# Kernel optimization log

Measured on AMD Instinct MI355X. Metric: run time of the kernel, lower is better.

Reference implementation:

```python
import jax, jax.numpy as jnp
import numpy as np

T_DEC = 60  # decoder steps, hard-coded in the original forward

def _conv1d(x, w, b):
    # x: [B, C_in, L], w: [C_out, C_in, K] -> [B, C_out, L-K+1] (valid conv)
    y = jax.lax.conv_general_dilated(x, w, window_strides=(1,), padding='VALID',
                                     dimension_numbers=('NCH', 'OIH', 'NCH'))
    return y + b[None, :, None]

def _lstm_cell(x, h, c, wih, whh, bih, bhh):
    # PyTorch LSTM cell, gate order i, f, g, o
    g = x @ wih.T + h @ whh.T + (bih + bhh)
    i, f, gg, o = jnp.split(g, 4, axis=-1)
    c = jax.nn.sigmoid(f) * c + jax.nn.sigmoid(i) * jnp.tanh(gg)
    h = jax.nn.sigmoid(o) * jnp.tanh(c)
    return h, c

def _lstm_seq(xs, wih, whh, bih, bhh, reverse=False):
    # xs: [B, T, D] -> [B, T, H], zero initial state (PyTorch default)
    B, H = xs.shape[0], whh.shape[1]
    xs_t = jnp.swapaxes(xs, 0, 1)
    if reverse:
        xs_t = xs_t[::-1]
    def step(carry, x):
        h, c = carry
        h, c = _lstm_cell(x, h, c, wih, whh, bih, bhh)
        return (h, c), h
    init = (jnp.zeros((B, H), xs.dtype), jnp.zeros((B, H), xs.dtype))
    _, hs = jax.lax.scan(step, init, xs_t)
    if reverse:
        hs = hs[::-1]
    return jnp.swapaxes(hs, 0, 1)

def setup_inputs():
    key = jax.random.key(0)
    B, L, D_in, H, D_out = 64, 4096, 64, 256, 128
    C1, C2, C3 = 8, 16, 32
    ks = jax.random.split(key, 32)
    it = iter(ks)
    def p(shape, scale=0.1):
        return jax.random.normal(next(it), shape, jnp.float32) * scale
    inp = {}
    inp['x'] = jax.random.normal(next(it), (B, L, D_in), jnp.float32)
    inp['conv_w1'] = p((C1, D_in, 4)); inp['conv_b1'] = p((C1,))
    inp['conv_w2'] = p((C2, C1, 8));  inp['conv_b2'] = p((C2,))
    inp['conv_w3'] = p((C3, C2, 16)); inp['conv_b3'] = p((C3,))
    inp['attn_w'] = p((H, C3)); inp['attn_b'] = p((H,))
    inp['dec1_wih'] = p((2, 4 * H, C3)); inp['dec1_whh'] = p((2, 4 * H, H))
    inp['dec1_bih'] = p((2, 4 * H));     inp['dec1_bhh'] = p((2, 4 * H))
    inp['dec2_wih0'] = p((2, 4 * H, 2 * H)); inp['dec2_whh0'] = p((2, 4 * H, H))
    inp['dec2_bih0'] = p((2, 4 * H));        inp['dec2_bhh0'] = p((2, 4 * H))
    inp['dec2_wih1'] = p((2, 4 * H, 2 * H)); inp['dec2_whh1'] = p((2, 4 * H, H))
    inp['dec2_bih1'] = p((2, 4 * H));        inp['dec2_bhh1'] = p((2, 4 * H))
    inp['out_w'] = p((D_out, 2 * H)); inp['out_b'] = p((D_out,))
    return inp

def reference(x, conv_w1, conv_b1, conv_w2, conv_b2, conv_w3, conv_b3,
              attn_w, attn_b, dec1_wih, dec1_whh, dec1_bih, dec1_bhh,
              dec2_wih0, dec2_whh0, dec2_bih0, dec2_bhh0,
              dec2_wih1, dec2_whh1, dec2_bih1, dec2_bhh1, out_w, out_b):
    # Eval mode: all dropouts are identity.
    h = jnp.swapaxes(x, 1, 2)  # [B, D_in, L]
    h = jax.nn.relu(_conv1d(h, conv_w1, conv_b1))
    h = jax.nn.relu(_conv1d(h, conv_w2, conv_b2))
    h = jax.nn.relu(_conv1d(h, conv_w3, conv_b3))
    enc = jnp.swapaxes(h, 1, 2)  # [B, Lp, 32], Lp = L - 25
    keys_t = jnp.einsum('blc,hc->bhl', enc, attn_w) + attn_b[None, :, None]  # [B, H, Lp]
    B, H = x.shape[0], attn_w.shape[0]

    def dec1(wih, whh, bih, bhh):
        def step(carry, _):
            hh, cc = carry
            align = jnp.einsum('bh,bhl->bl', hh, keys_t)   # attention scores over Lp
            a = jax.nn.softmax(align, axis=-1)
            ctx = jnp.einsum('bl,blc->bc', a, enc)         # context [B, 32]
            hh, cc = _lstm_cell(ctx, hh, cc, wih, whh, bih, bhh)
            return (hh, cc), hh
        init = (jnp.zeros((B, H), x.dtype), jnp.zeros((B, H), x.dtype))
        _, hs = jax.lax.scan(step, init, None, length=T_DEC)
        return jnp.swapaxes(hs, 0, 1)  # [B, 60, H]

    fwd = dec1(dec1_wih[0], dec1_whh[0], dec1_bih[0], dec1_bhh[0])
    # the bkwd branch writes step i into slot 60-i-1, i.e. time-reversed outputs
    bkwd = dec1(dec1_wih[1], dec1_whh[1], dec1_bih[1], dec1_bhh[1])[:, ::-1]
    d2in = jnp.concatenate([fwd, bkwd], axis=-1)  # [B, 60, 2H]
    l0 = jnp.concatenate([
        _lstm_seq(d2in, dec2_wih0[0], dec2_whh0[0], dec2_bih0[0], dec2_bhh0[0]),
        _lstm_seq(d2in, dec2_wih0[1], dec2_whh0[1], dec2_bih0[1], dec2_bhh0[1], reverse=True)], axis=-1)
    l1 = jnp.concatenate([
        _lstm_seq(l0, dec2_wih1[0], dec2_whh1[0], dec2_bih1[0], dec2_bhh1[0]),
        _lstm_seq(l0, dec2_wih1[1], dec2_whh1[1], dec2_bih1[1], dec2_bhh1[1], reverse=True)], axis=-1)
    return l1 @ out_w.T + out_b  # [B, 60, D_out]
```

## Files before the change

### kernel.cpp

```cpp
#include <hip/hip_runtime.h>

#define B_    64
#define L1C   4093
#define L2C   4086
#define L3C   4071
#define TDEC  60

static __device__ __forceinline__ float sigf(float x){ return 1.f/(1.f + __expf(-x)); }

typedef _Float16 h2_t __attribute__((ext_vector_type(2)));
union U2H { unsigned u; h2_t h; };

static __device__ __forceinline__ unsigned pkh2(float a, float b){
  U2H r; r.h[0] = (_Float16)a; r.h[1] = (_Float16)b; return r.u;
}
static __device__ __forceinline__ float dot2f(unsigned w, unsigned h, float acc){
  U2H a; a.u = w; U2H b; b.u = h;
#if __has_builtin(__builtin_amdgcn_fdot2)
  return __builtin_amdgcn_fdot2(a.h, b.h, acc, false);
#else
  acc = fmaf((float)a.h[0], (float)b.h[0], acc);
  acc = fmaf((float)a.h[1], (float)b.h[1], acc);
  return acc;
#endif
}

#define DOT8(g, wv, hv) \
  g = dot2f(wv.x, hv.x, g); g = dot2f(wv.y, hv.y, g); \
  g = dot2f(wv.z, hv.z, g); g = dot2f(wv.w, hv.w, g);

template<int CTRL>
static __device__ __forceinline__ float dppadd(float x){
  int y = __builtin_amdgcn_update_dpp(0, __float_as_int(x), CTRL, 0xf, 0xf, true);
  return x + __int_as_float(y);
}

template<int CIN,int COUT,int KW>
__global__ __launch_bounds__(256) void k_conv(
    const float* __restrict__ in, const float* __restrict__ w,
    const float* __restrict__ bias, float* __restrict__ outp,
    int Lin_, int Lout_)
{
  int g = blockIdx.x*256 + threadIdx.x;
  int bi = g / Lout_;
  int l  = g - bi*Lout_;
  if (bi >= B_) return;
  float acc[COUT];
#pragma unroll
  for (int o=0;o<COUT;o++) acc[o] = bias[o];
  const float* ip = in + ((size_t)bi*Lin_ + l)*CIN;
  for (int k=0;k<KW;k++){
#pragma unroll
    for (int i4=0;i4<CIN/4;i4++){
      float4 xv = *(const float4*)(ip + k*CIN + i4*4);
#pragma unroll
      for (int c=0;c<4;c++){
        float xs = (&xv.x)[c];
        int i = i4*4+c;
#pragma unroll
        for (int o=0;o<COUT;o++)
          acc[o] = fmaf(xs, w[(o*CIN + i)*KW + k], acc[o]);
      }
    }
  }
  float* op = outp + ((size_t)bi*Lout_ + l)*COUT;
#pragma unroll
  for (int o=0;o<COUT;o++) op[o] = fmaxf(acc[o],0.f);
}

__global__ __launch_bounds__(256) void k_conv3q(
    const float* __restrict__ in, const float* __restrict__ w,
    const float* __restrict__ bias, uint4* __restrict__ encq,
    float* __restrict__ encs, int Lin_, int Lout_)
{
  int g = blockIdx.x*256 + threadIdx.x;
  int bi = g / Lout_;
  int l  = g - bi*Lout_;
  if (bi >= B_) return;
  float acc[32];
#pragma unroll
  for (int o=0;o<32;o++) acc[o] = bias[o];
  const float* ip = in + ((size_t)bi*Lin_ + l)*16;
  for (int k=0;k<16;k++){
#pragma unroll
    for (int i4=0;i4<4;i4++){
      float4 xv = *(const float4*)(ip + k*16 + i4*4);
#pragma unroll
      for (int c=0;c<4;c++){
        float xs = (&xv.x)[c];
        int i = i4*4+c;
#pragma unroll
        for (int o=0;o<32;o++)
          acc[o] = fmaf(xs, w[(o*16 + i)*16 + k], acc[o]);
      }
    }
  }
  float mx = 0.f;
#pragma unroll
  for (int o=0;o<32;o++){ acc[o] = fmaxf(acc[o],0.f); mx = fmaxf(mx, acc[o]); }
  float scale = mx * (1.f/255.f);
  float inv = (mx > 0.f) ? (255.f/mx) : 0.f;
  unsigned qs[8];
#pragma unroll
  for (int q8=0;q8<8;q8++){
    unsigned q0 = (unsigned)(acc[q8*4+0]*inv + 0.5f);
    unsigned q1 = (unsigned)(acc[q8*4+1]*inv + 0.5f);
    unsigned q2 = (unsigned)(acc[q8*4+2]*inv + 0.5f);
    unsigned q3 = (unsigned)(acc[q8*4+3]*inv + 0.5f);
    qs[q8] = q0 | (q1<<8) | (q2<<16) | (q3<<24);
  }
  uint4* op = encq + ((size_t)bi*Lout_ + l)*2;
  op[0] = make_uint4(qs[0],qs[1],qs[2],qs[3]);
  op[1] = make_uint4(qs[4],qs[5],qs[6],qs[7]);
  encs[(size_t)bi*Lout_ + l] = scale;
}

__global__ __launch_bounds__(256) void k_packwh(
    const float* __restrict__ w, uint4* __restrict__ wT, int K)
{
  int gid = blockIdx.x*256 + threadIdx.x;
  int per = (K/8)*1024;
  int d = gid / per, rem = gid - d*per;
  int j8 = rem >> 10, row = rem & 1023;
  const float* src = w + ((size_t)d*1024 + row)*K + j8*8;
  float4 a = *(const float4*)src;
  float4 b = *(const float4*)(src+4);
  uint4 o;
  o.x = pkh2(a.x, a.y);
  o.y = pkh2(a.z, a.w);
  o.z = pkh2(b.x, b.y);
  o.w = pkh2(b.z, b.w);
  wT[gid] = o;
}

#define CVT8(r, qv) \
  r[0]=(float)( qv.x      & 255u); r[1]=(float)((qv.x>>8 ) & 255u); \
  r[2]=(float)((qv.x>>16) & 255u); r[3]=(float)((qv.x>>24)       ); \
  r[4]=(float)( qv.y      & 255u); r[5]=(float)((qv.y>>8 ) & 255u); \
  r[6]=(float)((qv.y>>16) & 255u); r[7]=(float)((qv.y>>24)       );

__global__ __launch_bounds__(1024) void k_dec1g(
    const uint4* __restrict__ encq,
    const float* __restrict__ encs,
    const float* __restrict__ attn_w,
    const uint4* __restrict__ wihT,
    const uint4* __restrict__ whhT,
    const float* __restrict__ bih, const float* __restrict__ bhh,
    float* __restrict__ d2in)
{
  int b = blockIdx.x, d = blockIdx.y, tid = threadIdx.x;
  int c = tid & 3, rb = tid >> 2;

  __shared__ __align__(16) uint2 encQ2[16384];
  __shared__ float sls[4096];
  __shared__ __align__(16) float hls[256];
  __shared__ __align__(16) unsigned h2pk[128];
  __shared__ __align__(16) unsigned ctxh[16];
  __shared__ float vl[32];
  __shared__ float maxenc[32];
  __shared__ float Msh;
  __shared__ float red[1024];
  __shared__ float scr[512];
  __shared__ float gls[1024];

  {
    const uint4* src = encq + (size_t)b*L3C*2;
    uint4* dst = (uint4*)encQ2;
    for (int i = tid; i < 8192; i += 1024)
      dst[i] = (i < L3C*2) ? src[i] : make_uint4(0,0,0,0);
    const float* ss = encs + (size_t)b*L3C;
    for (int i = tid; i < 4096; i += 1024)
      sls[i] = (i < L3C) ? ss[i] : 0.f;
  }
  if (tid < 256) hls[tid] = 0.f;
  if (tid < 128) h2pk[tid] = 0u;
  float creg = 0.f;
  float bsum = bih[(size_t)d*1024 + tid] + bhh[(size_t)d*1024 + tid];
  const uint4* whp = whhT + (size_t)d*32768;
  __syncthreads();

  {
    float mc[8];
#pragma unroll
    for (int j=0;j<8;j++) mc[j] = 0.f;
#pragma unroll
    for (int k=0;k<16;k++){
      int l = rb + 256*k;
      uint2 qv = encQ2[l*4 + c];
      float sl = sls[l];
      float r[8]; CVT8(r, qv)
#pragma unroll
      for (int j=0;j<8;j++) mc[j] = fmaxf(mc[j], r[j]*sl);
    }
#pragma unroll
    for (int off=4; off<=32; off<<=1){
#pragma unroll
      for (int j=0;j<8;j++) mc[j] = fmaxf(mc[j], __shfl_xor(mc[j], off));
    }
    int wid = tid >> 6;
    if ((tid&63) < 4){
#pragma unroll
      for (int j=0;j<8;j++) scr[wid*32 + c*8 + j] = mc[j];
    }
    __syncthreads();
    if (tid < 32){
      float mm = 0.f;
#pragma unroll
      for (int w=0;w<16;w++) mm = fmaxf(mm, scr[w*32 + tid]);
      maxenc[tid] = mm;
    }
    __syncthreads();
  }

  for (int t=0; t<TDEC; t++){
    {
      int cc = tid & 31, part = tid >> 5;
      const float* wp = attn_w + (size_t)(part*8)*32 + cc;
      float s = 0.f;
#pragma unroll
      for (int k=0;k<8;k++) s = fmaf(hls[part*8+k], wp[k*32], s);
      red[tid] = s;
    }
    __syncthreads();
    if (tid < 32){
      float v = 0.f;
#pragma unroll
      for (int q=0;q<32;q++) v += red[q*32 + tid];
      vl[tid] = v;
      float mt = maxenc[tid] * fmaxf(v, 0.f);
#pragma unroll
      for (int off=1; off<32; off<<=1) mt += __shfl_xor(mt, off);
      if (tid==0) Msh = mt;
    }
    __syncthreads();

    float vreg[8];
#pragma unroll
    for (int j=0;j<8;j++) vreg[j] = vl[c*8 + j];
    float M = Msh;
    float ssum = 0.f;
    float acc[8];
#pragma unroll
    for (int j=0;j<8;j++) acc[j] = 0.f;
    float g = bsum;
#pragma unroll 4
    for (int k=0;k<16;k++){
      uint4 wv0 = whp[(2*k  )*1024 + tid];
      uint4 wv1 = whp[(2*k+1)*1024 + tid];
      int l = rb + 256*k;
      uint2 qv = encQ2[l*4 + c];
      float sl = sls[l];
      float r[8]; CVT8(r, qv)
      float s = 0.f;
#pragma unroll
      for (int j=0;j<8;j++) s = fmaf(r[j], vreg[j], s);
      s = dppadd<0xB1>(s);
      s = dppadd<0x4E>(s);
      s *= sl;
      if (l >= L3C) s = -3.0e38f;
      float e = __expf(s - M);
      ssum += e;
      float em = e * sl;
#pragma unroll
      for (int j=0;j<8;j++) acc[j] = fmaf(em, r[j], acc[j]);
      uint4 hv0 = *(const uint4*)&h2pk[(2*k  )*4];
      uint4 hv1 = *(const uint4*)&h2pk[(2*k+1)*4];
      DOT8(g, wv0, hv0)
      DOT8(g, wv1, hv1)
    }
    ssum = dppadd<0x124>(ssum); ssum = dppadd<0x128>(ssum);
    ssum += __shfl_xor(ssum, 16); ssum += __shfl_xor(ssum, 32);
#pragma unroll
    for (int j=0;j<8;j++){
      acc[j] = dppadd<0x124>(acc[j]); acc[j] = dppadd<0x128>(acc[j]);
      acc[j] += __shfl_xor(acc[j], 16); acc[j] += __shfl_xor(acc[j], 32);
    }
    int wid = tid >> 6;
    if ((tid&63) < 4){
#pragma unroll
      for (int j=0;j<8;j++) scr[wid*32 + c*8 + j] = acc[j];
    }
    if ((tid&63)==0) red[wid] = ssum;
    __syncthreads();
    if (tid < 32){
      float S = 0.f, s2 = 0.f;
#pragma unroll
      for (int w=0;w<16;w++){ S += red[w]; s2 += scr[w*32 + tid]; }
      float cv = s2 / S;
      float co = __shfl_xor(cv, 1);
      if (!(tid&1)) ctxh[tid>>1] = pkh2(cv, co);
    }
    __syncthreads();

#pragma unroll
    for (int c8=0;c8<4;c8++){
      uint4 wv = wihT[(size_t)d*4096 + c8*1024 + tid];
      uint4 hv = *(const uint4*)&ctxh[c8*4];
      DOT8(g, wv, hv)
    }
    gls[tid] = g;
    __syncthreads();
    if (tid < 256){
      float ii = sigf(gls[tid]);
      float ff = sigf(gls[256+tid]);
      float gg = tanhf(gls[512+tid]);
      float oo = sigf(gls[768+tid]);
      creg = fmaf(ff, creg, ii*gg);
      float hn = oo * tanhf(creg);
      hls[tid] = hn;
      float ho = __shfl_xor(hn, 1);
      if (!(tid&1)) h2pk[tid>>1] = pkh2(hn, ho);
      int tout = d ? (59 - t) : t;
      d2in[((size_t)b*60 + tout)*512 + d*256 + tid] = hn;
    }
    __syncthreads();
  }
}

__global__ __launch_bounds__(256) void k_gemm(
    const float* __restrict__ A, const float* __restrict__ W,
    float* __restrict__ C, const float* __restrict__ b1, const float* __restrict__ b2,
    int K, int ldc, size_t sW, size_t sC, int sB)
{
  int m0 = blockIdx.x * 128, n0 = blockIdx.y * 128, z = blockIdx.z;
  const float* Wz = W + (size_t)z*sW;
  float* Cz = C + (size_t)z*sC;
  const float* b1z = b1 + (size_t)z*sB;
  const float* b2z = b2 ? (b2 + (size_t)z*sB) : nullptr;
  __shared__ __align__(16) float As[16][132];
  __shared__ __align__(16) float Bs[16][132];
  int tid = threadIdx.x;
  int tx = tid & 15, ty = tid >> 4;
  int r = tid >> 2, c4 = tid & 3;
  float acc[8][8] = {};
  for (int k0=0; k0<K; k0+=16){
#pragma unroll
    for (int h=0; h<2; h++){
      int rr = r + h*64;
      float4 av = *(const float4*)(A  + (size_t)(m0+rr)*K + k0 + c4*4);
      float4 bv = *(const float4*)(Wz + (size_t)(n0+rr)*K + k0 + c4*4);
      As[c4*4+0][rr]=av.x; As[c4*4+1][rr]=av.y; As[c4*4+2][rr]=av.z; As[c4*4+3][rr]=av.w;
      Bs[c4*4+0][rr]=bv.x; Bs[c4*4+1][rr]=bv.y; Bs[c4*4+2][rr]=bv.z; Bs[c4*4+3][rr]=bv.w;
    }
    __syncthreads();
#pragma unroll
    for (int kk=0; kk<16; kk++){
      float a[8], bb[8];
      *(float4*)&a[0]  = *(const float4*)&As[kk][ty*8];
      *(float4*)&a[4]  = *(const float4*)&As[kk][ty*8+4];
      *(float4*)&bb[0] = *(const float4*)&Bs[kk][tx*8];
      *(float4*)&bb[4] = *(const float4*)&Bs[kk][tx*8+4];
#pragma unroll
      for (int i=0;i<8;i++)
#pragma unroll
        for (int j=0;j<8;j++)
          acc[i][j] = fmaf(a[i], bb[j], acc[i][j]);
    }
    __syncthreads();
  }
  float bb1[8];
#pragma unroll
  for (int j=0;j<8;j++){
    int n = n0 + tx*8 + j;
    bb1[j] = b1z[n] + (b2z ? b2z[n] : 0.f);
  }
#pragma unroll
  for (int i=0;i<8;i++){
    int m = m0 + ty*8 + i;
    float o[8];
#pragma unroll
    for (int j=0;j<8;j++) o[j] = acc[i][j] + bb1[j];
    *(float4*)(Cz + (size_t)m*ldc + n0 + tx*8)     = *(const float4*)&o[0];
    *(float4*)(Cz + (size_t)m*ldc + n0 + tx*8 + 4) = *(const float4*)&o[4];
  }
}

__global__ __launch_bounds__(1024) void k_rec2(
    const float* __restrict__ xg,
    const uint4* __restrict__ wT,
    float* __restrict__ out)
{
  int b = blockIdx.x, d = blockIdx.y, tid = threadIdx.x;
  __shared__ __align__(16) unsigned h2pk[128];
  __shared__ float gls[1024];
  float c = 0.f;
  if (tid < 128) h2pk[tid] = 0u;
  const uint4* wp = wT + (size_t)d*32*1024;
  uint4 wpre[16];
#pragma unroll
  for (int j=0;j<16;j++) wpre[j] = wp[j*1024 + tid];
  const float* xp = xg + (((size_t)d*64 + b)*60)*1024;
  __syncthreads();
  for (int step=0; step<TDEC; step++){
    int t = d ? (TDEC-1-step) : step;
    float g = xp[(size_t)t*1024 + tid];
#pragma unroll
    for (int j8=0;j8<16;j8++){
      uint4 hv = *(const uint4*)&h2pk[j8*4];
      DOT8(g, wpre[j8], hv)
    }
#pragma unroll 4
    for (int j8=16;j8<32;j8++){
      uint4 wv = wp[j8*1024 + tid];
      uint4 hv = *(const uint4*)&h2pk[j8*4];
      DOT8(g, wv, hv)
    }
    gls[tid] = g;
    __syncthreads();
    if (tid < 256){
      float ii = sigf(gls[tid]);
      float ff = sigf(gls[256+tid]);
      float gg = tanhf(gls[512+tid]);
      float oo = sigf(gls[768+tid]);
      c = fmaf(ff, c, ii*gg);
      float hn = oo * tanhf(c);
      float ho = __shfl_xor(hn, 1);
      if (!(tid&1)) h2pk[tid>>1] = pkh2(hn, ho);
      out[((size_t)b*60 + t)*512 + d*256 + tid] = hn;
    }
    __syncthreads();
  }
}

extern "C" void kernel_launch(void* const* d_in, const int* in_sizes, int n_in,
                              void* d_out, int out_size, void* d_ws, size_t ws_size,
                              hipStream_t stream) {
  const float* x      = (const float*)d_in[0];
  const float* cw1    = (const float*)d_in[1];
  const float* cb1    = (const float*)d_in[2];
  const float* cw2    = (const float*)d_in[3];
  const float* cb2    = (const float*)d_in[4];
  const float* cw3    = (const float*)d_in[5];
  const float* cb3    = (const float*)d_in[6];
  const float* attn_w = (const float*)d_in[7];
  const float* d1_wih = (const float*)d_in[9];
  const float* d1_whh = (const float*)d_in[10];
  const float* d1_bih = (const float*)d_in[11];
  const float* d1_bhh = (const float*)d_in[12];
  const float* w2_ih0 = (const float*)d_in[13];
  const float* w2_hh0 = (const float*)d_in[14];
  const float* b2_ih0 = (const float*)d_in[15];
  const float* b2_hh0 = (const float*)d_in[16];
  const float* w2_ih1 = (const float*)d_in[17];
  const float* w2_hh1 = (const float*)d_in[18];
  const float* b2_ih1 = (const float*)d_in[19];
  const float* b2_hh1 = (const float*)d_in[20];
  const float* out_w  = (const float*)d_in[21];
  const float* out_b  = (const float*)d_in[22];

  char* ws = (char*)d_ws;
  size_t off = 0;
  uint4* encq = (uint4*)(ws + off);
  float* encs = (float*)(ws + off + 8338432);
  off += 16675840;
  size_t off_h1 = off;
  float* h1buf = (float*)(ws + off); off += 8382464;
  float* h2buf = (float*)(ws + off); off += 16736256;
  float* d2in  = (float*)(ws + off_h1);
  float* l0    = (float*)(ws + off_h1 + 7864320);
  float* l1    = (float*)(ws + off_h1 + 15728640);
  uint4* wT    = (uint4*)(ws + off_h1 + 23592960);
  float* xg    = (float*)(ws + off); off += 31457280;
  uint4* d1whhT = (uint4*)xg;
  uint4* d1wihT = (uint4*)((char*)xg + 1048576);
  (void)ws_size; (void)in_sizes; (void)n_in; (void)out_size;

  k_packwh<<<256,256,0,stream>>>(d1_whh, d1whhT, 256);
  k_packwh<<<32, 256,0,stream>>>(d1_wih, d1wihT, 32);

  int g1 = (B_*L1C + 255)/256;
  k_conv<64,8,4><<<g1,256,0,stream>>>(x, cw1, cb1, h1buf, 4096, L1C);
  int g2 = (B_*L2C + 255)/256;
  k_conv<8,16,8><<<g2,256,0,stream>>>(h1buf, cw2, cb2, h2buf, L1C, L2C);
  int g3 = (B_*L3C + 255)/256;
  k_conv3q<<<g3,256,0,stream>>>(h2buf, cw3, cb3, encq, encs, L2C, L3C);

  k_dec1g<<<dim3(64,2),1024,0,stream>>>(encq, encs, attn_w, d1wihT, d1whhT,
                                        d1_bih, d1_bhh, d2in);

  k_packwh<<<256,256,0,stream>>>(w2_hh0, wT, 256);
  k_gemm<<<dim3(30,8,2),256,0,stream>>>(d2in, w2_ih0, xg, b2_ih0, b2_hh0,
                                        512, 1024, (size_t)1024*512, (size_t)3840*1024, 1024);
  k_rec2<<<dim3(64,2),1024,0,stream>>>(xg, wT, l0);
  k_packwh<<<256,256,0,stream>>>(w2_hh1, wT, 256);
  k_gemm<<<dim3(30,8,2),256,0,stream>>>(l0, w2_ih1, xg, b2_ih1, b2_hh1,
                                        512, 1024, (size_t)1024*512, (size_t)3840*1024, 1024);
  k_rec2<<<dim3(64,2),1024,0,stream>>>(xg, wT, l1);
  k_gemm<<<dim3(30,1,1),256,0,stream>>>(l1, out_w, (float*)d_out, out_b, nullptr,
                                        512, 128, 0, 0, 0);
}
```

Baseline: 1.606 ms.

## Stage conv input windows in shared memory and preload more recurrent weights

The three conv kernels now launch one block per (batch, 256-position tile). Each block first loads its input window plus halo into padded shared memory, and each thread then reads its overlapping receptive field from LDS instead of re-reading global memory per tap. Separately, the layer-2 recurrent kernel keeps 20 of its 32 weight chunks in registers instead of 16, which cuts global weight reloads per step but raises register pressure at 1024 threads per block.

```diff
diff --git a/kernel.cpp b/kernel.cpp
--- a/kernel.cpp
+++ b/kernel.cpp
@@ -35,64 +35,72 @@
   return x + __int_as_float(y);
 }
 
-template<int CIN,int COUT,int KW>
-__global__ __launch_bounds__(256) void k_conv(
+template<int CIN,int COUT,int KW,int CINP>
+__global__ __launch_bounds__(256) void k_convL(
     const float* __restrict__ in, const float* __restrict__ w,
     const float* __restrict__ bias, float* __restrict__ outp,
     int Lin_, int Lout_)
 {
-  int g = blockIdx.x*256 + threadIdx.x;
-  int bi = g / Lout_;
-  int l  = g - bi*Lout_;
-  if (bi >= B_) return;
+  __shared__ float xs[(256+KW-1)*CINP];
+  int bi = blockIdx.y, l0 = blockIdx.x*256, tid = threadIdx.x;
+  int nrow = min(256+KW-1, Lin_-l0);
+  const float* ip = in + ((size_t)bi*Lin_ + l0)*CIN;
+  for (int i = tid; i < nrow*(CIN/4); i += 256){
+    int rr = i/(CIN/4), cc = i - rr*(CIN/4);
+    float4 v = *(const float4*)(ip + rr*CIN + cc*4);
+    float* dst = &xs[rr*CINP + cc*4];
+    dst[0]=v.x; dst[1]=v.y; dst[2]=v.z; dst[3]=v.w;
+  }
+  __syncthreads();
+  int l = l0 + tid;
+  if (l >= Lout_) return;
   float acc[COUT];
 #pragma unroll
   for (int o=0;o<COUT;o++) acc[o] = bias[o];
-  const float* ip = in + ((size_t)bi*Lin_ + l)*CIN;
   for (int k=0;k<KW;k++){
-#pragma unroll
-    for (int i4=0;i4<CIN/4;i4++){
-      float4 xv = *(const float4*)(ip + k*CIN + i4*4);
-#pragma unroll
-      for (int c=0;c<4;c++){
-        float xs = (&xv.x)[c];
-        int i = i4*4+c;
-#pragma unroll
-        for (int o=0;o<COUT;o++)
-          acc[o] = fmaf(xs, w[(o*CIN + i)*KW + k], acc[o]);
-      }
+    const float* xr = &xs[(tid+k)*CINP];
+#pragma unroll
+    for (int i=0;i<CIN;i++){
+      float xv = xr[i];
+#pragma unroll
+      for (int o=0;o<COUT;o++)
+        acc[o] = fmaf(xv, w[(o*CIN + i)*KW + k], acc[o]);
     }
   }
   float* op = outp + ((size_t)bi*Lout_ + l)*COUT;
 #pragma unroll
-  for (int o=0;o<COUT;o++) op[o] = fmaxf(acc[o],0.f);
-}
-
-__global__ __launch_bounds__(256) void k_conv3q(
+  for (int o=0;o<COUT;o++) op[o] = fmaxf(acc[o], 0.f);
+}
+
+__global__ __launch_bounds__(256) void k_conv3qL(
     const float* __restrict__ in, const float* __restrict__ w,
     const float* __restrict__ bias, uint4* __restrict__ encq,
     float* __restrict__ encs, int Lin_, int Lout_)
 {
-  int g = blockIdx.x*256 + threadIdx.x;
-  int bi = g / Lout_;
-  int l  = g - bi*Lout_;
-  if (bi >= B_) return;
+  __shared__ float xs[(256+15)*17];
+  int bi = blockIdx.y, l0 = blockIdx.x*256, tid = threadIdx.x;
+  int nrow = min(256+15, Lin_-l0);
+  const float* ip = in + ((size_t)bi*Lin_ + l0)*16;
+  for (int i = tid; i < nrow*4; i += 256){
+    int rr = i>>2, cc = i&3;
+    float4 v = *(const float4*)(ip + rr*16 + cc*4);
+    float* dst = &xs[rr*17 + cc*4];
+    dst[0]=v.x; dst[1]=v.y; dst[2]=v.z; dst[3]=v.w;
+  }
+  __syncthreads();
+  int l = l0 + tid;
+  if (l >= Lout_) return;
   float acc[32];
 #pragma unroll
   for (int o=0;o<32;o++) acc[o] = bias[o];
-  const float* ip = in + ((size_t)bi*Lin_ + l)*16;
   for (int k=0;k<16;k++){
-#pragma unroll
-    for (int i4=0;i4<4;i4++){
-      float4 xv = *(const float4*)(ip + k*16 + i4*4);
-#pragma unroll
-      for (int c=0;c<4;c++){
-        float xs = (&xv.x)[c];
-        int i = i4*4+c;
-#pragma unroll
-        for (int o=0;o<32;o++)
-          acc[o] = fmaf(xs, w[(o*16 + i)*16 + k], acc[o]);
-      }
+    const float* xr = &xs[(tid+k)*17];
+#pragma unroll
+    for (int i=0;i<16;i++){
+      float xv = xr[i];
+#pragma unroll
+      for (int o=0;o<32;o++)
+        acc[o] = fmaf(xv, w[(o*16 + i)*16 + k], acc[o]);
     }
   }
   float mx = 0.f;
@@ -386,21 +394,21 @@
   float c = 0.f;
   if (tid < 128) h2pk[tid] = 0u;
   const uint4* wp = wT + (size_t)d*32*1024;
-  uint4 wpre[16];
-#pragma unroll
-  for (int j=0;j<16;j++) wpre[j] = wp[j*1024 + tid];
+  uint4 wpre[20];
+#pragma unroll
+  for (int j=0;j<20;j++) wpre[j] = wp[j*1024 + tid];
   const float* xp = xg + (((size_t)d*64 + b)*60)*1024;
   __syncthreads();
   for (int step=0; step<TDEC; step++){
     int t = d ? (TDEC-1-step) : step;
     float g = xp[(size_t)t*1024 + tid];
 #pragma unroll
-    for (int j8=0;j8<16;j8++){
+    for (int j8=0;j8<20;j8++){
       uint4 hv = *(const uint4*)&h2pk[j8*4];
       DOT8(g, wpre[j8], hv)
     }
 #pragma unroll 4
-    for (int j8=16;j8<32;j8++){
+    for (int j8=20;j8<32;j8++){
       uint4 wv = wp[j8*1024 + tid];
       uint4 hv = *(const uint4*)&h2pk[j8*4];
       DOT8(g, wv, hv)
@@ -468,12 +476,9 @@
   k_packwh<<<256,256,0,stream>>>(d1_whh, d1whhT, 256);
   k_packwh<<<32, 256,0,stream>>>(d1_wih, d1wihT, 32);
 
-  int g1 = (B_*L1C + 255)/256;
-  k_conv<64,8,4><<<g1,256,0,stream>>>(x, cw1, cb1, h1buf, 4096, L1C);
-  int g2 = (B_*L2C + 255)/256;
-  k_conv<8,16,8><<<g2,256,0,stream>>>(h1buf, cw2, cb2, h2buf, L1C, L2C);
-  int g3 = (B_*L3C + 255)/256;
-  k_conv3q<<<g3,256,0,stream>>>(h2buf, cw3, cb3, encq, encs, L2C, L3C);
+  k_convL<64,8,4,65><<<dim3(16,B_),256,0,stream>>>(x, cw1, cb1, h1buf, 4096, L1C);
+  k_convL<8,16,8,9><<<dim3(16,B_),256,0,stream>>>(h1buf, cw2, cb2, h2buf, L1C, L2C);
+  k_conv3qL<<<dim3(16,B_),256,0,stream>>>(h2buf, cw3, cb3, encq, encs, L2C, L3C);
 
   k_dec1g<<<dim3(64,2),1024,0,stream>>>(encq, encs, attn_w, d1wihT, d1whhT,
                                         d1_bih, d1_bhh, d2in);
```

Result: no change. 1.616 ms (+0.6%).
